# Optimization experiments

Hardware: AMD Instinct MI355X
Metric: run time of the kernel (lower is better)

The kernel has to match this reference:

```python
import jax, jax.numpy as jnp
import numpy as np


def squash(s, axis=-1):
    sq = jnp.sum(jnp.square(s), axis=axis, keepdims=True)
    scale = sq / (1.0 + sq) / (jnp.sqrt(sq) + 1e-08)
    return scale * s


def setup_inputs() -> dict:
    key = jax.random.key(0)
    k1, k2 = jax.random.split(key)
    # [B, input_num_caps, input_dim_caps]
    x = jax.random.normal(k1, (64, 1152, 8), dtype=jnp.float32)
    # W: [input_num_caps, num_capsules, input_dim_caps, dim_capsules]
    W = jax.random.normal(k2, (1152, 32, 8, 16), dtype=jnp.float32) * 0.05
    return {"x": x, "W": W}


def reference(x, W):
    # Original tiles x along the output-capsule axis before the einsum
    # 'bicd,icde->bice'; since the tiled copies are identical along c,
    # this is exactly 'bid,icde->bice' without materializing the tile.
    u_hat = jnp.einsum('bid,icde->bice', x, W)  # [B, I, C, E]
    b = jnp.zeros(u_hat.shape[:3], dtype=u_hat.dtype)  # [B, I, C]
    routings = 3
    v = None
    for i in range(routings):
        c = jax.nn.softmax(b, axis=-1)                 # over output capsules
        s = jnp.einsum('bic,bice->bce', c, u_hat)      # weighted sum over I
        v = squash(s)                                  # [B, C, E]
        if i < routings - 1:
            b = b + jnp.einsum('bice,bce->bic', u_hat, v)  # agreement
    return v
```

## Files before the change

### kernel.cpp

```cpp
#include <hip/hip_runtime.h>
#include <hip/hip_fp16.h>

#define B_ 64
#define I_ 1152
#define C_ 32
#define E_ 16
#define D_ 8
#define BC_ 8
#define ICt 12
#define NIC (I_/ICt)
#define ICX (NIC/8)
#define SCE (B_*C_*E_)
#define SCE2 (SCE/2)
#define WIB 8192

__device__ __forceinline__ void gload_lds16(const void* g, void* l) {
  typedef __attribute__((address_space(1))) const void GV;
  typedef __attribute__((address_space(3))) void LV;
  __builtin_amdgcn_global_load_lds((GV*)g, (LV*)l, 16, 0, 0);
}

#define WAITVM8() do { asm volatile("s_waitcnt vmcnt(8)" ::: "memory"); \
                       __builtin_amdgcn_sched_barrier(0); } while (0)
#define WAITVM4() do { asm volatile("s_waitcnt vmcnt(4)" ::: "memory"); \
                       __builtin_amdgcn_sched_barrier(0); } while (0)
#define WAITVM0() do { asm volatile("s_waitcnt vmcnt(0)" ::: "memory"); \
                       __builtin_amdgcn_sched_barrier(0); } while (0)
#define WAITLG0() do { asm volatile("s_waitcnt lgkmcnt(0)" ::: "memory"); \
                       __builtin_amdgcn_sched_barrier(0); } while (0)

typedef _Float16 h2v __attribute__((ext_vector_type(2)));

__device__ __forceinline__ float dot2f(__half2 a, __half2 b, float c) {
#if defined(__has_builtin)
#if __has_builtin(__builtin_amdgcn_fdot2)
  return __builtin_amdgcn_fdot2(__builtin_bit_cast(h2v, a),
                                __builtin_bit_cast(h2v, b), c, false);
#else
  float2 fa = __half22float2(a), fb = __half22float2(b);
  return fmaf(fa.x, fb.x, fmaf(fa.y, fb.y, c));
#endif
#else
  float2 fa = __half22float2(a), fb = __half22float2(b);
  return fmaf(fa.x, fb.x, fmaf(fa.y, fb.y, c));
#endif
}

__global__ __launch_bounds__(256)
void convert_wx(const float* __restrict__ W, const float* __restrict__ x,
                __half* __restrict__ Wh, __half2* __restrict__ xh)
{
  const int bid = blockIdx.x;
  const int t   = threadIdx.x;
  if (bid < 2304) {
    int G = bid*256 + t;
    const float4* src = (const float4*)(W + (size_t)G*8);
    float4 a = src[0], b = src[1];
    __half2 h0 = __float22half2_rn({a.x, a.y});
    __half2 h1 = __float22half2_rn({a.z, a.w});
    __half2 h2 = __float22half2_rn({b.x, b.y});
    __half2 h3 = __float22half2_rn({b.z, b.w});
    float4 o;
    o.x = __builtin_bit_cast(float, h0); o.y = __builtin_bit_cast(float, h1);
    o.z = __builtin_bit_cast(float, h2); o.w = __builtin_bit_cast(float, h3);
    *(float4*)(Wh + (size_t)G*8) = o;
  } else {
    int k = (bid - 2304)*256 + t;
    const float4* src = (const float4*)(x + (size_t)k*4);
    float4 a = src[0];
    float4 o;
    o.x = __builtin_bit_cast(float, __float22half2_rn({a.x, a.x}));
    o.y = __builtin_bit_cast(float, __float22half2_rn({a.y, a.y}));
    o.z = __builtin_bit_cast(float, __float22half2_rn({a.z, a.z}));
    o.w = __builtin_bit_cast(float, __float22half2_rn({a.w, a.w}));
    *(float4*)(xh + (size_t)k*4) = o;
  }
}

template<bool ROUTE>
__global__ __launch_bounds__(256)
void caps_pass(const __half2* __restrict__ xh, const char* __restrict__ Wh,
               const float* __restrict__ vacc, __half* __restrict__ partial)
{
  __shared__ float4 Wl[3][1024];
  __shared__ __half2 xl[BC_*ICt*D_];

  const int t   = threadIdx.x;
  const int c   = t & 31;
  const int eh  = (t >> 5) & 1;
  const int bq  = t >> 6;
  const int xcd = blockIdx.x & 7;
  const int sl  = blockIdx.x >> 3;
  const int ic  = xcd * ICX + (sl >> 3);
  const int b0  = (sl & 7) * BC_;
  const int i0  = ic * ICt;

  int fsrc[2];
#pragma unroll
  for (int k = 0; k < 2; ++k) {
    int g = t + 256*k, cc = g >> 4, q = g & 15;
    fsrc[k] = cc*256 + ((q ^ (cc & 15)) << 4);
  }

  __half2 vrp[2][4];
  if (ROUTE) {
#pragma unroll
    for (int j = 0; j < 2; ++j) {
      const float4* vp = (const float4*)(vacc + (((size_t)(b0 + bq*2 + j)*C_ + c)*E_ + eh*8));
      float4 a = vp[0], b = vp[1];
      vrp[j][0] = __float22half2_rn({a.x, a.y});
      vrp[j][1] = __float22half2_rn({a.z, a.w});
      vrp[j][2] = __float22half2_rn({b.x, b.y});
      vrp[j][3] = __float22half2_rn({b.z, b.w});
    }
  }

  if (t < BC_*ICt*D_/4) {
    int b = t / 24, r = t % 24;
    float4 v = ((const float4*)(xh + ((size_t)(b0 + b)*I_ + i0)*D_))[r];
    ((float4*)xl)[b*24 + r] = v;
  }

  const char* wg = Wh + (size_t)i0 * WIB;
#pragma unroll
  for (int k = 0; k < 4; ++k)
    gload_lds16(wg + (k>>1)*WIB + fsrc[k&1], (char*)&Wl[0][0] + (t + 256*k)*16);
#pragma unroll
  for (int k = 0; k < 4; ++k)
    gload_lds16(wg + WIB*2 + (k>>1)*WIB + fsrc[k&1], (char*)&Wl[1][0] + (t + 256*k)*16);

  __half2 accp[2][4];
#pragma unroll
  for (int j = 0; j < 2; ++j)
#pragma unroll
    for (int q = 0; q < 4; ++q) accp[j][q] = __half2{__half(0.f), __half(0.f)};

  int cur = 0;
  for (int p = 0; p < ICt/2; ++p) {
    WAITLG0();
    __builtin_amdgcn_s_barrier();
    __builtin_amdgcn_sched_barrier(0);

    if (p + 2 < ICt/2) {
      int pre = cur + 2; if (pre >= 3) pre -= 3;
      const char* wn = wg + (size_t)(p + 2) * (2*WIB);
#pragma unroll
      for (int k = 0; k < 4; ++k)
        gload_lds16(wn + (k>>1)*WIB + fsrc[k&1], (char*)&Wl[pre][0] + (t + 256*k)*16);
    }

    if (p < ICt/2 - 2)       WAITVM8();
    else if (p == ICt/2 - 2) WAITVM4();
    else                     WAITVM0();
    __builtin_amdgcn_s_barrier();
    __builtin_amdgcn_sched_barrier(0);

#pragma unroll
    for (int il = 0; il < 2; ++il) {
      const int ii = p*2 + il;

      __half2 xd0[8], xd1[8];
      {
        const float4* xr = (const float4*)xl;
        float4 a0 = xr[((bq*2 + 0)*ICt + ii)*2 + 0];
        float4 b0v = xr[((bq*2 + 0)*ICt + ii)*2 + 1];
        float4 a1 = xr[((bq*2 + 1)*ICt + ii)*2 + 0];
        float4 b1v = xr[((bq*2 + 1)*ICt + ii)*2 + 1];
        xd0[0]=__builtin_bit_cast(__half2,a0.x); xd0[1]=__builtin_bit_cast(__half2,a0.y);
        xd0[2]=__builtin_bit_cast(__half2,a0.z); xd0[3]=__builtin_bit_cast(__half2,a0.w);
        xd0[4]=__builtin_bit_cast(__half2,b0v.x); xd0[5]=__builtin_bit_cast(__half2,b0v.y);
        xd0[6]=__builtin_bit_cast(__half2,b0v.z); xd0[7]=__builtin_bit_cast(__half2,b0v.w);
        xd1[0]=__builtin_bit_cast(__half2,a1.x); xd1[1]=__builtin_bit_cast(__half2,a1.y);
        xd1[2]=__builtin_bit_cast(__half2,a1.z); xd1[3]=__builtin_bit_cast(__half2,a1.w);
        xd1[4]=__builtin_bit_cast(__half2,b1v.x); xd1[5]=__builtin_bit_cast(__half2,b1v.y);
        xd1[6]=__builtin_bit_cast(__half2,b1v.z); xd1[7]=__builtin_bit_cast(__half2,b1v.w);
      }

      __half2 uhp[2][4];
#pragma unroll
      for (int j = 0; j < 2; ++j)
#pragma unroll
        for (int q = 0; q < 4; ++q) uhp[j][q] = __half2{__half(0.f), __half(0.f)};

      const char* wrow = (const char*)&Wl[cur][0] + il*WIB + c*256;
#pragma unroll
      for (int d = 0; d < D_; ++d) {
        float4 w4 = *(const float4*)(wrow + ((((d*2 + eh) ^ (c & 15))) << 4));
        __half2 w0 = __builtin_bit_cast(__half2, w4.x);
        __half2 w1 = __builtin_bit_cast(__half2, w4.y);
        __half2 w2 = __builtin_bit_cast(__half2, w4.z);
        __half2 w3 = __builtin_bit_cast(__half2, w4.w);
        uhp[0][0] = __hfma2(xd0[d], w0, uhp[0][0]);
        uhp[0][1] = __hfma2(xd0[d], w1, uhp[0][1]);
        uhp[0][2] = __hfma2(xd0[d], w2, uhp[0][2]);
        uhp[0][3] = __hfma2(xd0[d], w3, uhp[0][3]);
        uhp[1][0] = __hfma2(xd1[d], w0, uhp[1][0]);
        uhp[1][1] = __hfma2(xd1[d], w1, uhp[1][1]);
        uhp[1][2] = __hfma2(xd1[d], w2, uhp[1][2]);
        uhp[1][3] = __hfma2(xd1[d], w3, uhp[1][3]);
      }

      float coef[2];
      if (ROUTE) {
#pragma unroll
        for (int j = 0; j < 2; ++j) {
          float lg = 0.f;
#pragma unroll
          for (int q = 0; q < 4; ++q) lg = dot2f(uhp[j][q], vrp[j][q], lg);
          lg += __shfl_xor(lg, 32, 64);
          float pexp = __expf(lg);
          float s = pexp;
#pragma unroll
          for (int mk = 16; mk >= 1; mk >>= 1) s += __shfl_xor(s, mk, 64);
          coef[j] = pexp * __builtin_amdgcn_rcpf(s);
        }
      } else {
#pragma unroll
        for (int j = 0; j < 2; ++j) coef[j] = (1.0f / C_);
      }

#pragma unroll
      for (int j = 0; j < 2; ++j) {
        __half2 cp = __float2half2_rn(coef[j]);
#pragma unroll
        for (int q = 0; q < 4; ++q) accp[j][q] = __hfma2(cp, uhp[j][q], accp[j][q]);
      }
    }

    cur = (cur + 1 == 3) ? 0 : cur + 1;
  }

#pragma unroll
  for (int j = 0; j < 2; ++j) {
    size_t base = ((size_t)ic * B_ + (b0 + bq*2 + j)) * (C_*E_) + (size_t)c*E_ + eh*8;
    float4 o;
    o.x = __builtin_bit_cast(float, accp[j][0]);
    o.y = __builtin_bit_cast(float, accp[j][1]);
    o.z = __builtin_bit_cast(float, accp[j][2]);
    o.w = __builtin_bit_cast(float, accp[j][3]);
    *(float4*)(partial + base) = o;
  }
}

__global__ __launch_bounds__(256)
void reduce_squash(const __half2* __restrict__ partial, float* __restrict__ vacc,
                   float* __restrict__ out, int mode)
{
  __shared__ float2 sm[256];
  const int t    = threadIdx.x;
  const int pair = blockIdx.x*32 + (t & 31);
  const int part = t >> 5;
  const __half2* p = partial + (size_t)(part*(NIC/8)) * SCE2 + pair;
  float2 s = {0.f, 0.f};
#pragma unroll
  for (int k = 0; k < NIC/8; ++k) {
    float2 f = __half22float2(p[(size_t)k * SCE2]);
    s.x += f.x; s.y += f.y;
  }
  sm[t] = s;
  __syncthreads();
  if (t < 32) {
    float2 tot = {0.f, 0.f};
#pragma unroll
    for (int pp = 0; pp < 8; ++pp) {
      float2 v = sm[t + 32*pp];
      tot.x += v.x; tot.y += v.y;
    }
    float sq = tot.x*tot.x + tot.y*tot.y;
    sq += __shfl_xor(sq, 1); sq += __shfl_xor(sq, 2); sq += __shfl_xor(sq, 4);
    float scale = sq / (1.f + sq) / (sqrtf(sq) + 1e-8f);
    float vx = scale * tot.x, vy = scale * tot.y;
    const int cell = pair * 2;
    if (mode == 0)      { vacc[cell] = vx;  vacc[cell+1] = vy;  }
    else if (mode == 1) { vacc[cell] += vx; vacc[cell+1] += vy; }
    else                { out[cell]  = vx;  out[cell+1]  = vy;  }
  }
}

extern "C" void kernel_launch(void* const* d_in, const int* in_sizes, int n_in,
                              void* d_out, int out_size, void* d_ws, size_t ws_size,
                              hipStream_t stream)
{
  const float* x = (const float*)d_in[0];
  const float* W = (const float*)d_in[1];
  float* out     = (float*)d_out;

  char* ws = (char*)d_ws;
  __half*  partial = (__half*)ws;                    ws += (size_t)NIC*SCE*2;
  float*   vacc    = (float*)ws;                     ws += (size_t)SCE*4;
  __half*  Wh      = (__half*)ws;                    ws += (size_t)I_*C_*D_*E_*2;
  __half2* xh      = (__half2*)ws;

  dim3 pg(NIC * (B_/BC_));
  const int rg = SCE2 / 32;

  convert_wx<<<2880, 256, 0, stream>>>(W, x, Wh, xh);

  caps_pass<false><<<pg, 256, 0, stream>>>(xh, (const char*)Wh, nullptr, partial);
  reduce_squash<<<rg, 256, 0, stream>>>((const __half2*)partial, vacc, nullptr, 0);
  caps_pass<true ><<<pg, 256, 0, stream>>>(xh, (const char*)Wh, vacc, partial);
  reduce_squash<<<rg, 256, 0, stream>>>((const __half2*)partial, vacc, nullptr, 1);
  caps_pass<true ><<<pg, 256, 0, stream>>>(xh, (const char*)Wh, vacc, partial);
  reduce_squash<<<rg, 256, 0, stream>>>((const __half2*)partial, vacc, out, 2);
}
```

Baseline: 73.55 us.

## Fuse fp16 conversion of W and x into first routing pass

Removes the separate convert kernel and makes the first routing pass read fp32 W and x directly, computing with fp32 FMAs from an LDS-staged, rotated layout. While doing so it writes the fp16 copies of W and x for the later passes. It also raises wave priority around the compute sections with s_setprio. The intent is to save one launch and one full pass over W. The cost is a heavier first pass with twice the LDS traffic per W row and extra global writes at its end.

```diff
diff --git a/kernel.cpp b/kernel.cpp
--- a/kernel.cpp
+++ b/kernel.cpp
@@ -10,6 +10,7 @@
 #define ICt 12
 #define NIC (I_/ICt)
 #define ICX (NIC/8)
+#define WROW4 (C_*D_*E_/4)
 #define SCE (B_*C_*E_)
 #define SCE2 (SCE/2)
 #define WIB 8192
@@ -46,41 +47,156 @@
 #endif
 }
 
+__device__ __forceinline__ float h2bits(float a, float b) {
+  return __builtin_bit_cast(float, __float22half2_rn({a, b}));
+}
+
 __global__ __launch_bounds__(256)
-void convert_wx(const float* __restrict__ W, const float* __restrict__ x,
-                __half* __restrict__ Wh, __half2* __restrict__ xh)
+void caps_pass0(const float* __restrict__ x, const float* __restrict__ W,
+                __half* __restrict__ partial, __half* __restrict__ Wh,
+                __half2* __restrict__ xh)
 {
-  const int bid = blockIdx.x;
-  const int t   = threadIdx.x;
-  if (bid < 2304) {
-    int G = bid*256 + t;
-    const float4* src = (const float4*)(W + (size_t)G*8);
-    float4 a = src[0], b = src[1];
-    __half2 h0 = __float22half2_rn({a.x, a.y});
-    __half2 h1 = __float22half2_rn({a.z, a.w});
-    __half2 h2 = __float22half2_rn({b.x, b.y});
-    __half2 h3 = __float22half2_rn({b.z, b.w});
+  __shared__ float4 Wl[3][1024];
+  __shared__ float4 xl[BC_*ICt*2];
+
+  const int t     = threadIdx.x;
+  const int c     = t & 31;
+  const int eh    = (t >> 5) & 1;
+  const int bq    = t >> 6;
+  const int xcd   = blockIdx.x & 7;
+  const int sl    = blockIdx.x >> 3;
+  const int ic    = xcd * ICX + (sl >> 3);
+  const int bslab = sl & 7;
+  const int b0    = bslab * BC_;
+  const int i0    = ic * ICt;
+
+  int fsrc[4];
+#pragma unroll
+  for (int k = 0; k < 4; ++k) {
+    int cc = (t >> 5) + 8*k;
+    fsrc[k] = cc*32 + ((c - cc) & 31);
+  }
+
+  if (t < BC_*ICt*2) {
+    int b = t / (ICt*2), r = t % (ICt*2);
+    xl[t] = ((const float4*)x)[ ((size_t)(b0 + b)*I_ + i0)*2 + r ];
+  }
+
+  const float4* wg = (const float4*)(W + (size_t)i0 * (C_*D_*E_));
+#pragma unroll
+  for (int k = 0; k < 4; ++k) gload_lds16(wg + fsrc[k],          &Wl[0][t + 256*k]);
+#pragma unroll
+  for (int k = 0; k < 4; ++k) gload_lds16(wg + WROW4 + fsrc[k],  &Wl[1][t + 256*k]);
+
+  float acc[2][8];
+#pragma unroll
+  for (int j = 0; j < 2; ++j)
+#pragma unroll
+    for (int e = 0; e < 8; ++e) acc[j][e] = 0.f;
+
+  int cur = 0;
+  for (int ii = 0; ii < ICt; ++ii) {
+    WAITLG0();
+    __builtin_amdgcn_s_barrier();
+    __builtin_amdgcn_sched_barrier(0);
+
+    if (ii + 2 < ICt) {
+      int pre = cur + 2; if (pre >= 3) pre -= 3;
+      const float4* wn = wg + (size_t)(ii + 2) * WROW4;
+#pragma unroll
+      for (int k = 0; k < 4; ++k)
+        gload_lds16(wn + fsrc[k], &Wl[pre][t + 256*k]);
+    }
+
+    if (ii < ICt - 2)       WAITVM8();
+    else if (ii == ICt - 2) WAITVM4();
+    else                    WAITVM0();
+    __builtin_amdgcn_s_barrier();
+    __builtin_amdgcn_sched_barrier(0);
+
+    __builtin_amdgcn_s_setprio(1);
+    float xv[2][8];
+#pragma unroll
+    for (int j = 0; j < 2; ++j) {
+      float4 a = xl[(bq*2 + j)*(ICt*2) + ii*2 + 0];
+      float4 b = xl[(bq*2 + j)*(ICt*2) + ii*2 + 1];
+      xv[j][0]=a.x; xv[j][1]=a.y; xv[j][2]=a.z; xv[j][3]=a.w;
+      xv[j][4]=b.x; xv[j][5]=b.y; xv[j][6]=b.z; xv[j][7]=b.w;
+    }
+
+    float uh[2][8];
+#pragma unroll
+    for (int j = 0; j < 2; ++j)
+#pragma unroll
+      for (int e = 0; e < 8; ++e) uh[j][e] = 0.f;
+
+#pragma unroll
+    for (int d = 0; d < D_; ++d) {
+#pragma unroll
+      for (int qq = 0; qq < 2; ++qq) {
+        float4 wv = Wl[cur][c*32 + (((d*4 + eh*2 + qq) + c) & 31)];
+        const int eb = qq*4;
+#pragma unroll
+        for (int j = 0; j < 2; ++j) {
+          uh[j][eb+0] = fmaf(xv[j][d], wv.x, uh[j][eb+0]);
+          uh[j][eb+1] = fmaf(xv[j][d], wv.y, uh[j][eb+1]);
+          uh[j][eb+2] = fmaf(xv[j][d], wv.z, uh[j][eb+2]);
+          uh[j][eb+3] = fmaf(xv[j][d], wv.w, uh[j][eb+3]);
+        }
+      }
+    }
+
+#pragma unroll
+    for (int j = 0; j < 2; ++j)
+#pragma unroll
+      for (int e = 0; e < 8; ++e) acc[j][e] = fmaf((1.0f/C_), uh[j][e], acc[j][e]);
+    __builtin_amdgcn_s_setprio(0);
+
+    cur = (cur + 1 == 3) ? 0 : cur + 1;
+  }
+
+#pragma unroll
+  for (int j = 0; j < 2; ++j) {
+    size_t base = ((size_t)ic * B_ + (b0 + bq*2 + j)) * (C_*E_) + (size_t)c*E_ + eh*8;
     float4 o;
-    o.x = __builtin_bit_cast(float, h0); o.y = __builtin_bit_cast(float, h1);
-    o.z = __builtin_bit_cast(float, h2); o.w = __builtin_bit_cast(float, h3);
-    *(float4*)(Wh + (size_t)G*8) = o;
-  } else {
-    int k = (bid - 2304)*256 + t;
-    const float4* src = (const float4*)(x + (size_t)k*4);
-    float4 a = src[0];
+    o.x = h2bits(acc[j][0], acc[j][1]);
+    o.y = h2bits(acc[j][2], acc[j][3]);
+    o.z = h2bits(acc[j][4], acc[j][5]);
+    o.w = h2bits(acc[j][6], acc[j][7]);
+    *(float4*)(partial + base) = o;
+  }
+
+  for (int ii = bslab; ii < ICt; ii += 8) {
+    const int i = i0 + ii;
+    const float4* src = (const float4*)(W + (size_t)i * (C_*D_*E_));
+#pragma unroll
+    for (int g = 0; g < 2; ++g) {
+      int G  = t*2 + g;
+      int cc = G >> 4, q = G & 15;
+      int d  = q >> 1, eo = q & 1;
+      const float4* s4 = src + (cc*8 + d)*4 + eo*2;
+      float4 a = s4[0], b = s4[1];
+      float4 o;
+      o.x = h2bits(a.x, a.y); o.y = h2bits(a.z, a.w);
+      o.z = h2bits(b.x, b.y); o.w = h2bits(b.z, b.w);
+      *(float4*)(Wh + (size_t)i * 4096 + G*8) = o;
+    }
+  }
+  if (t < BC_*ICt*2) {
+    int b = t / (ICt*2), r = t % (ICt*2);
+    float4 a = xl[t];
     float4 o;
-    o.x = __builtin_bit_cast(float, __float22half2_rn({a.x, a.x}));
-    o.y = __builtin_bit_cast(float, __float22half2_rn({a.y, a.y}));
-    o.z = __builtin_bit_cast(float, __float22half2_rn({a.z, a.z}));
-    o.w = __builtin_bit_cast(float, __float22half2_rn({a.w, a.w}));
-    *(float4*)(xh + (size_t)k*4) = o;
-  }
-}
-
-template<bool ROUTE>
+    o.x = h2bits(a.x, a.x); o.y = h2bits(a.y, a.y);
+    o.z = h2bits(a.z, a.z); o.w = h2bits(a.w, a.w);
+    size_t idx = ((size_t)(b0 + b)*I_ + (i0 + (r >> 1)))*D_ + (r & 1)*4;
+    *(float4*)(xh + idx) = o;
+  }
+}
+
+template<int MODE>
 __global__ __launch_bounds__(256)
-void caps_pass(const __half2* __restrict__ xh, const char* __restrict__ Wh,
-               const float* __restrict__ vacc, __half* __restrict__ partial)
+void caps_pass_f16(const __half2* __restrict__ xh, const char* __restrict__ Wh,
+                   const float* __restrict__ vacc, __half* __restrict__ partial)
 {
   __shared__ float4 Wl[3][1024];
   __shared__ __half2 xl[BC_*ICt*D_];
@@ -103,16 +219,14 @@
   }
 
   __half2 vrp[2][4];
-  if (ROUTE) {
-#pragma unroll
-    for (int j = 0; j < 2; ++j) {
-      const float4* vp = (const float4*)(vacc + (((size_t)(b0 + bq*2 + j)*C_ + c)*E_ + eh*8));
-      float4 a = vp[0], b = vp[1];
-      vrp[j][0] = __float22half2_rn({a.x, a.y});
-      vrp[j][1] = __float22half2_rn({a.z, a.w});
-      vrp[j][2] = __float22half2_rn({b.x, b.y});
-      vrp[j][3] = __float22half2_rn({b.z, b.w});
-    }
+#pragma unroll
+  for (int j = 0; j < 2; ++j) {
+    const float4* vp = (const float4*)(vacc + (((size_t)(b0 + bq*2 + j)*C_ + c)*E_ + eh*8));
+    float4 a = vp[0], b = vp[1];
+    vrp[j][0] = __float22half2_rn({a.x, a.y});
+    vrp[j][1] = __float22half2_rn({a.z, a.w});
+    vrp[j][2] = __float22half2_rn({b.x, b.y});
+    vrp[j][3] = __float22half2_rn({b.z, b.w});
   }
 
   if (t < BC_*ICt*D_/4) {
@@ -155,6 +269,7 @@
     __builtin_amdgcn_s_barrier();
     __builtin_amdgcn_sched_barrier(0);
 
+    __builtin_amdgcn_s_setprio(1);
 #pragma unroll
     for (int il = 0; il < 2; ++il) {
       const int ii = p*2 + il;
@@ -201,22 +316,17 @@
       }
 
       float coef[2];
-      if (ROUTE) {
-#pragma unroll
-        for (int j = 0; j < 2; ++j) {
-          float lg = 0.f;
-#pragma unroll
-          for (int q = 0; q < 4; ++q) lg = dot2f(uhp[j][q], vrp[j][q], lg);
-          lg += __shfl_xor(lg, 32, 64);
-          float pexp = __expf(lg);
-          float s = pexp;
-#pragma unroll
-          for (int mk = 16; mk >= 1; mk >>= 1) s += __shfl_xor(s, mk, 64);
-          coef[j] = pexp * __builtin_amdgcn_rcpf(s);
-        }
-      } else {
-#pragma unroll
-        for (int j = 0; j < 2; ++j) coef[j] = (1.0f / C_);
+#pragma unroll
+      for (int j = 0; j < 2; ++j) {
+        float lg = 0.f;
+#pragma unroll
+        for (int q = 0; q < 4; ++q) lg = dot2f(uhp[j][q], vrp[j][q], lg);
+        lg += __shfl_xor(lg, 32, 64);
+        float pexp = __expf(lg);
+        float s = pexp;
+#pragma unroll
+        for (int mk = 16; mk >= 1; mk >>= 1) s += __shfl_xor(s, mk, 64);
+        coef[j] = pexp * __builtin_amdgcn_rcpf(s);
       }
 
 #pragma unroll
@@ -226,6 +336,7 @@
         for (int q = 0; q < 4; ++q) accp[j][q] = __hfma2(cp, uhp[j][q], accp[j][q]);
       }
     }
+    __builtin_amdgcn_s_setprio(0);
 
     cur = (cur + 1 == 3) ? 0 : cur + 1;
   }
@@ -294,12 +405,10 @@
   dim3 pg(NIC * (B_/BC_));
   const int rg = SCE2 / 32;
 
-  convert_wx<<<2880, 256, 0, stream>>>(W, x, Wh, xh);
-
-  caps_pass<false><<<pg, 256, 0, stream>>>(xh, (const char*)Wh, nullptr, partial);
+  caps_pass0<<<pg, 256, 0, stream>>>(x, W, partial, Wh, xh);
   reduce_squash<<<rg, 256, 0, stream>>>((const __half2*)partial, vacc, nullptr, 0);
-  caps_pass<true ><<<pg, 256, 0, stream>>>(xh, (const char*)Wh, vacc, partial);
+  caps_pass_f16<0><<<pg, 256, 0, stream>>>(xh, (const char*)Wh, vacc, partial);
   reduce_squash<<<rg, 256, 0, stream>>>((const __half2*)partial, vacc, nullptr, 1);
-  caps_pass<true ><<<pg, 256, 0, stream>>>(xh, (const char*)Wh, vacc, partial);
+  caps_pass_f16<1><<<pg, 256, 0, stream>>>(xh, (const char*)Wh, vacc, partial);
   reduce_squash<<<rg, 256, 0, stream>>>((const __half2*)partial, vacc, out, 2);
 }
```

Measured after the change: 65.96 us (median of 2 runs). 1.12x faster.
